# Kernel optimization log

Hardware: AMD Instinct MI355X
Metric: run time of the kernel (lower is better)

Reference implementation:

```python
import jax, jax.numpy as jnp
import numpy as np

B, S, D, H = 2, 2048, 1024, 16
HD = D // H               # head_dim = input_size / num_heads
STEPS = 1                 # update_steps_max extra Hopfield update steps
LN_EPS = 1e-5
SCALING = 1.0 / np.sqrt(HD)  # beta = 1/sqrt(head_dim)


def layernorm(x, g, b):
    m = x.mean(-1, keepdims=True)
    v = ((x - m) ** 2).mean(-1, keepdims=True)
    return (x - m) * jax.lax.rsqrt(v + LN_EPS) * g + b


def setup_inputs() -> dict:
    key = jax.random.key(0)
    ks = jax.random.split(key, 9)
    s = 0.02
    f32 = jnp.float32
    return {
        "data": jax.random.normal(ks[0], (B, S, D), f32),
        # affine LayerNorm params (stored / state / projection patterns)
        "g_k": jnp.ones((D,), f32), "b_k": jnp.zeros((D,), f32),
        "g_q": jnp.ones((D,), f32), "b_q": jnp.zeros((D,), f32),
        "g_v": jnp.ones((D,), f32), "b_v": jnp.zeros((D,), f32),
        # in-projections (q/k/v) and out-projection of HopfieldCore
        "Wq": jax.random.normal(ks[1], (D, D), f32) * s, "bq": jnp.zeros((D,), f32),
        "Wk": jax.random.normal(ks[2], (D, D), f32) * s, "bk": jnp.zeros((D,), f32),
        "Wv": jax.random.normal(ks[3], (D, D), f32) * s, "bv": jnp.zeros((D,), f32),
        "Wo": jax.random.normal(ks[4], (D, D), f32) * s, "bo": jnp.zeros((D,), f32),
    }


def reference(data, g_k, b_k, g_q, b_q, g_v, b_v,
              Wq, bq, Wk, bk, Wv, bv, Wo, bo):
    # single input tensor used as stored / state / projection pattern
    xk = layernorm(data, g_k, b_k)   # stored pattern  -> keys
    xq = layernorm(data, g_q, b_q)   # state pattern   -> queries
    xv = layernorm(data, g_v, b_v)   # pattern proj    -> values

    split = lambda t: t.reshape(B, S, H, HD).transpose(0, 2, 1, 3)  # [B,H,S,HD]
    q = split(xq @ Wq + bq)
    k = split(xk @ Wk + bk)
    v = split(xv @ Wv + bv)

    def assoc(q):  # xi = softmax(beta * q K^T)
        return jax.nn.softmax(
            jnp.einsum('bhqd,bhkd->bhqk', q, k) * SCALING, axis=-1)

    xi = assoc(q)
    for _ in range(STEPS):           # iterative Hopfield update: q <- xi K
        q = jnp.einsum('bhqk,bhkd->bhqd', xi, k)
        xi = assoc(q)

    out = jnp.einsum('bhqk,bhkd->bhqd', xi, v)        # retrieve with values
    out = out.transpose(0, 2, 1, 3).reshape(B, S, D)  # merge heads
    return out @ Wo + bo
```

## Files before the change

kernel.cpp:

```cpp
#include <hip/hip_runtime.h>
#include <hip/hip_bf16.h>

#define B_  2
#define S_  2048
#define D_  1024
#define H_  16
#define HD_ 64
#define M_  4096


typedef __attribute__((ext_vector_type(8))) short short8;
typedef __attribute__((ext_vector_type(4))) float f32x4;
typedef __attribute__((ext_vector_type(16))) float f32x16;

#define CE_ 0.1803368801111204f

typedef __attribute__((address_space(1))) const unsigned GU;
typedef __attribute__((address_space(3))) unsigned LU;
static __device__ __forceinline__ void glds16(const void* g, void* l){
  __builtin_amdgcn_global_load_lds((GU*)g, (LU*)l, 16, 0, 0);
}

static __device__ __forceinline__ unsigned short f2bfc(float f){
  union{float f; unsigned u;} c; c.f = f;
  return (unsigned short)((c.u + 0x8000u) >> 16);
}
static __device__ __forceinline__ unsigned pk2bf(float a, float b){
  union{float f; unsigned u;} ca, cb; ca.f=a; cb.f=b;
  return __builtin_amdgcn_perm(cb.u + 0x8000u, ca.u + 0x8000u, 0x07060302u);
}
static __device__ __forceinline__ unsigned pk2bft(float a, float b){
  union{float f; unsigned u;} ca, cb; ca.f=a; cb.f=b;
  return __builtin_amdgcn_perm(cb.u, ca.u, 0x07060302u);
}
static __device__ __forceinline__ short8 mk8(unsigned x0, unsigned x1,
                                             unsigned x2, unsigned x3){
  union{ unsigned u[4]; short8 s; } t;
  t.u[0]=x0; t.u[1]=x1; t.u[2]=x2; t.u[3]=x3; return t.s;
}
static __device__ __forceinline__ void plswap(unsigned &x, unsigned &y){
  auto r = __builtin_amdgcn_permlane32_swap(x, y, false, false);
  x = (unsigned)r[0]; y = (unsigned)r[1];
}

__global__ __launch_bounds__(256) void prep_kernel(
  const float* __restrict__ data,
  const float* __restrict__ Wq, const float* __restrict__ Wk,
  const float* __restrict__ Wv, const float* __restrict__ Wo,
  const float* __restrict__ gq, const float* __restrict__ gk, const float* __restrict__ gv,
  const float* __restrict__ blq, const float* __restrict__ blk, const float* __restrict__ blv,
  const float* __restrict__ bpq, const float* __restrict__ bpk, const float* __restrict__ bpv,
  unsigned short* __restrict__ WT, unsigned short* __restrict__ xhat,
  float* __restrict__ bf)
{
  __shared__ unsigned short tile[64][72];
  __shared__ float red[4][64];
  int bid = blockIdx.x, t = threadIdx.x;
  if (bid < 1024){
    int z = bid >> 8, rem = bid & 255;
    int k0 = (rem>>4)*64, n0 = (rem&15)*64;
    const float* W = (z==0)?Wq:(z==1)?Wk:(z==2)?Wv:Wo;
    const float* g = (z==0)?gq:(z==1)?gk:(z==2)?gv:(const float*)0;
    unsigned short* out = WT + ((size_t)z<<20);
    {
      int kr = t>>2, c16 = (t&3)*16;
      float gs = g ? g[k0+kr]*((z==0)?CE_:1.0f) : 1.0f;
      const float* src = W + (size_t)(k0+kr)*D_ + n0 + c16;
      float4 w0 = *(const float4*)(src);
      float4 w1 = *(const float4*)(src+4);
      float4 w2 = *(const float4*)(src+8);
      float4 w3 = *(const float4*)(src+12);
      unsigned* tp = (unsigned*)&tile[kr][c16];
      tp[0]=pk2bf(w0.x*gs,w0.y*gs); tp[1]=pk2bf(w0.z*gs,w0.w*gs);
      tp[2]=pk2bf(w1.x*gs,w1.y*gs); tp[3]=pk2bf(w1.z*gs,w1.w*gs);
      tp[4]=pk2bf(w2.x*gs,w2.y*gs); tp[5]=pk2bf(w2.z*gs,w2.w*gs);
      tp[6]=pk2bf(w3.x*gs,w3.y*gs); tp[7]=pk2bf(w3.z*gs,w3.w*gs);
    }
    __syncthreads();
    {
      int nr = t>>2, kc = (t&3)*16;
      union { uint4 v[2]; unsigned short u[16]; } st;
      #pragma unroll
      for (int i=0;i<16;i++) st.u[i] = tile[kc+i][nr];
      unsigned short* dst = out + (size_t)(n0+nr)*D_ + k0 + kc;
      *(uint4*)(dst)     = st.v[0];
      *(uint4*)(dst + 8) = st.v[1];
    }
  } else if (bid < 2048){
    int row = (bid-1024)*4 + (t>>6);
    int l = t & 63;
    const float4* xr = (const float4*)(data + (size_t)row*D_);
    float4 v[4];
    float s = 0.f, ss = 0.f;
    #pragma unroll
    for (int i=0;i<4;i++){
      v[i] = xr[l + 64*i];
      s  += v[i].x+v[i].y+v[i].z+v[i].w;
      ss += v[i].x*v[i].x+v[i].y*v[i].y+v[i].z*v[i].z+v[i].w*v[i].w;
    }
    #pragma unroll
    for (int m=1;m<64;m<<=1){ s += __shfl_xor(s, m, 64); ss += __shfl_xor(ss, m, 64); }
    float me = s*(1.0f/D_);
    float var = ss*(1.0f/D_) - me*me;
    float rs = rsqrtf(var + 1e-5f);
    float nm = -me*rs;
    unsigned short* xo = xhat + (size_t)row*D_;
    #pragma unroll
    for (int i=0;i<4;i++){
      uint2 pk;
      pk.x = pk2bf(fmaf(v[i].x,rs,nm), fmaf(v[i].y,rs,nm));
      pk.y = pk2bf(fmaf(v[i].z,rs,nm), fmaf(v[i].w,rs,nm));
      *(uint2*)(xo + 4*l + 256*i) = pk;
    }
  } else {
    int idx = bid - 2048;
    int z = idx >> 4, xb = idx & 15;
    const float* W  = (z==0)?Wq:(z==1)?Wk:Wv;
    const float* bl = (z==0)?blq:(z==1)?blk:blv;
    const float* bp = (z==0)?bpq:(z==1)?bpk:bpv;
    int nl = t & 63, kg = t >> 6;
    int n = xb*64 + nl;
    float acc = 0.f;
    for (int k = kg*256; k < (kg+1)*256; k++)
      acc += bl[k] * W[(size_t)k*D_ + n];
    red[kg][nl] = acc;
    __syncthreads();
    if (t < 64){
      int nn = xb*64 + t;
      float v = red[0][t]+red[1][t]+red[2][t]+red[3][t] + bp[nn];
      bf[z*D_ + nn] = (z==0) ? v*CE_ : v;
    }
  }
}

__global__ __launch_bounds__(256) void gemm_qkv(
  const unsigned short* __restrict__ xhat,
  const unsigned short* __restrict__ WT,
  const float* __restrict__ biasf,
  unsigned short* __restrict__ qv, unsigned short* __restrict__ kb,
  unsigned short* __restrict__ kT, unsigned short* __restrict__ vT)
{
  int z = blockIdx.z;
  const unsigned short* Bt = WT + ((size_t)z<<20);
  const float* bias = biasf + z*D_;
  unsigned short* oN = (z==0)?qv:(z==1)?kb:(unsigned short*)0;
  unsigned short* oT = (z==0)?(unsigned short*)0:(z==1)?kT:vT;

  __shared__ __align__(16) unsigned short As[128*32];
  __shared__ __align__(16) unsigned short Bs[128*32];
  int tid = threadIdx.x, w = tid>>6, l = tid&63;
  int m0 = blockIdx.x*128, n0 = blockIdx.y*128;
  int wr = (w>>1)*64, wc = (w&1)*64;
  int lr = l&15, qd = l>>4;

  const unsigned short* gA = xhat + (size_t)(m0 + w*32 + (l>>2))*D_ + (l&3)*8;
  const unsigned short* gB = Bt   + (size_t)(n0 + w*32 + (l>>2))*D_ + (l&3)*8;
  unsigned short* lA0 = &As[(w*32)*32];
  unsigned short* lA1 = &As[(w*32+16)*32];
  unsigned short* lB0 = &Bs[(w*32)*32];
  unsigned short* lB1 = &Bs[(w*32+16)*32];

  const f32x4 fz = {0.f,0.f,0.f,0.f};
  f32x4 acc[4][4];
  #pragma unroll
  for (int i=0;i<4;i++)
    #pragma unroll
    for (int j=0;j<4;j++) acc[i][j] = fz;

  for (int kk=0; kk<D_; kk+=32){
    __syncthreads();
    glds16(gA + kk,                 lA0);
    glds16(gA + kk + (size_t)16*D_, lA1);
    glds16(gB + kk,                 lB0);
    glds16(gB + kk + (size_t)16*D_, lB1);
    __syncthreads();
    short8 af[4], bfr[4];
    #pragma unroll
    for (int i=0;i<4;i++) af[i]  = *(const short8*)(As + (wr + i*16 + lr)*32 + qd*8);
    #pragma unroll
    for (int j=0;j<4;j++) bfr[j] = *(const short8*)(Bs + (wc + j*16 + lr)*32 + qd*8);
    #pragma unroll
    for (int i=0;i<4;i++)
      #pragma unroll
      for (int j=0;j<4;j++)
        acc[i][j] = __builtin_amdgcn_mfma_f32_16x16x32_bf16(af[i], bfr[j], acc[i][j], 0, 0, 0);
  }

  #pragma unroll
  for (int j=0;j<4;j++){
    int n = n0 + wc + j*16 + lr;
    float bias_n = bias[n];
    #pragma unroll
    for (int i=0;i<4;i++){
      int mb = m0 + wr + i*16 + qd*4;
      float v0 = acc[i][j][0] + bias_n;
      float v1 = acc[i][j][1] + bias_n;
      float v2 = acc[i][j][2] + bias_n;
      float v3 = acc[i][j][3] + bias_n;
      if (oN){
        oN[(size_t)(mb+0)*D_ + n] = f2bfc(v0);
        oN[(size_t)(mb+1)*D_ + n] = f2bfc(v1);
        oN[(size_t)(mb+2)*D_ + n] = f2bfc(v2);
        oN[(size_t)(mb+3)*D_ + n] = f2bfc(v3);
      }
      if (oT){
        int bb = mb >> 11, sI = mb & (S_-1);
        int hh = n >> 6,  dd = n & 63;
        uint2 pk; pk.x = pk2bf(v0, v1); pk.y = pk2bf(v2, v3);
        *(uint2*)(oT + (size_t)((bb*H_ + hh)*HD_ + dd)*S_ + sI) = pk;
      }
    }
  }
}

__global__ __launch_bounds__(256) void gemm_out(
  const unsigned short* __restrict__ A,
  const unsigned short* __restrict__ Bt,
  const float* __restrict__ bo,
  float* __restrict__ Cf)
{
  __shared__ __align__(16) unsigned short As[128*32];
  __shared__ __align__(16) unsigned short Bs[128*32];
  int tid = threadIdx.x, w = tid>>6, l = tid&63;
  int m0 = blockIdx.x*128, n0 = blockIdx.y*128;
  int wr = (w>>1)*64, wc = (w&1)*64;
  int lr = l&15, qd = l>>4;

  const unsigned short* gA = A  + (size_t)(m0 + w*32 + (l>>2))*D_ + (l&3)*8;
  const unsigned short* gB = Bt + (size_t)(n0 + w*32 + (l>>2))*D_ + (l&3)*8;
  unsigned short* lA0 = &As[(w*32)*32];
  unsigned short* lA1 = &As[(w*32+16)*32];
  unsigned short* lB0 = &Bs[(w*32)*32];
  unsigned short* lB1 = &Bs[(w*32+16)*32];

  const f32x4 fz = {0.f,0.f,0.f,0.f};
  f32x4 acc[4][4];
  #pragma unroll
  for (int i=0;i<4;i++)
    #pragma unroll
    for (int j=0;j<4;j++) acc[i][j] = fz;

  for (int kk=0; kk<D_; kk+=32){
    __syncthreads();
    glds16(gA + kk,                 lA0);
    glds16(gA + kk + (size_t)16*D_, lA1);
    glds16(gB + kk,                 lB0);
    glds16(gB + kk + (size_t)16*D_, lB1);
    __syncthreads();
    short8 af[4], bfr[4];
    #pragma unroll
    for (int i=0;i<4;i++) af[i]  = *(const short8*)(As + (wr + i*16 + lr)*32 + qd*8);
    #pragma unroll
    for (int j=0;j<4;j++) bfr[j] = *(const short8*)(Bs + (wc + j*16 + lr)*32 + qd*8);
    #pragma unroll
    for (int i=0;i<4;i++)
      #pragma unroll
      for (int j=0;j<4;j++)
        acc[i][j] = __builtin_amdgcn_mfma_f32_16x16x32_bf16(af[i], bfr[j], acc[i][j], 0, 0, 0);
  }

  #pragma unroll
  for (int j=0;j<4;j++){
    int n = n0 + wc + j*16 + lr;
    float bias_n = bo[n];
    #pragma unroll
    for (int i=0;i<4;i++){
      int mb = m0 + wr + i*16 + qd*4;
      Cf[(size_t)(mb+0)*D_ + n] = acc[i][j][0] + bias_n;
      Cf[(size_t)(mb+1)*D_ + n] = acc[i][j][1] + bias_n;
      Cf[(size_t)(mb+2)*D_ + n] = acc[i][j][2] + bias_n;
      Cf[(size_t)(mb+3)*D_ + n] = acc[i][j][3] + bias_n;
    }
  }
}

__global__ __launch_bounds__(256) void attn_fused(
  unsigned short* __restrict__ QO,
  const unsigned short* __restrict__ K,
  const unsigned short* __restrict__ KT,
  const unsigned short* __restrict__ VT)
{
  int qt = blockIdx.x;
  int h  = blockIdx.y;
  int b  = qt >> 4;
  int bh = b*H_ + h;
  int tid = threadIdx.x, w = tid>>6, l = tid&63;
  int lq = l & 31;
  int hi = l >> 5;
  int r8 = tid>>3, c8 = (tid&7)*8;
  int swzw = (r8&7)<<3;
  int swzr = (lq&7)<<3;

  __shared__ __align__(16) unsigned short sK[64*64];
  __shared__ __align__(16) unsigned short sV[64*64];

  const f32x16 fz16 = {0.f,0.f,0.f,0.f,0.f,0.f,0.f,0.f,
                       0.f,0.f,0.f,0.f,0.f,0.f,0.f,0.f};
  const short8 ones = {(short)0x3F80,(short)0x3F80,(short)0x3F80,(short)0x3F80,
                       (short)0x3F80,(short)0x3F80,(short)0x3F80,(short)0x3F80};

  const unsigned short* Qb = QO + (size_t)(qt*128 + w*32 + lq)*D_ + h*64;
  short8 qf[4];
  #pragma unroll
  for (int d=0; d<4; d++)
    qf[d] = *(const short8*)(Qb + d*16 + hi*8);

  const unsigned short* Khead = K + (size_t)(b*S_)*D_ + h*64;
  const unsigned short* Vh0 = KT + (size_t)bh*HD_*S_;
  const unsigned short* Vh1 = VT + (size_t)bh*HD_*S_;

  uint4 kr0, kr1, vr0, vr1;
  kr0 = *(const uint4*)(Khead + (size_t)(r8   )*D_ + c8);
  kr1 = *(const uint4*)(Khead + (size_t)(r8+32)*D_ + c8);
  vr0 = *(const uint4*)(Vh0 + (size_t)(r8   )*S_ + c8);
  vr1 = *(const uint4*)(Vh0 + (size_t)(r8+32)*S_ + c8);

  #pragma unroll 1
  for (int phase=0; phase<2; phase++){
    const unsigned short* Vhead = phase ? Vh1 : Vh0;
    f32x16 oacc0 = fz16, oacc1 = fz16, lacc = fz16;

    for (int kt=0; kt<S_; kt+=64){
      __syncthreads();
      *(uint4*)(&sK[(size_t)(r8   )*64 + (c8 ^ swzw)]) = kr0;
      *(uint4*)(&sK[(size_t)(r8+32)*64 + (c8 ^ swzw)]) = kr1;
      *(uint4*)(&sV[(size_t)(r8   )*64 + (c8 ^ swzw)]) = vr0;
      *(uint4*)(&sV[(size_t)(r8+32)*64 + (c8 ^ swzw)]) = vr1;
      __syncthreads();

      {
        int nkt = kt + 64;
        const unsigned short* Vn = Vhead;
        if (nkt >= S_){ nkt = 0; Vn = Vh1; }
        kr0 = *(const uint4*)(Khead + (size_t)(nkt+r8   )*D_ + c8);
        kr1 = *(const uint4*)(Khead + (size_t)(nkt+r8+32)*D_ + c8);
        vr0 = *(const uint4*)(Vn + (size_t)(r8   )*S_ + nkt + c8);
        vr1 = *(const uint4*)(Vn + (size_t)(r8+32)*S_ + nkt + c8);
      }

      f32x16 sc0 = fz16, sc1 = fz16;
      #pragma unroll
      for (int ds_=0; ds_<4; ds_++){
        short8 ka0 = *(const short8*)(&sK[(size_t)(lq   )*64 + ((ds_*16 + hi*8) ^ swzr)]);
        short8 ka1 = *(const short8*)(&sK[(size_t)(lq+32)*64 + ((ds_*16 + hi*8) ^ swzr)]);
        sc0 = __builtin_amdgcn_mfma_f32_32x32x16_bf16(ka0, qf[ds_], sc0, 0,0,0);
        sc1 = __builtin_amdgcn_mfma_f32_32x32x16_bf16(ka1, qf[ds_], sc1, 0,0,0);
      }

      float p0[16], p1[16];
      #pragma unroll
      for (int i=0;i<16;i++){
        p0[i] = __builtin_amdgcn_exp2f(sc0[i]);
        p1[i] = __builtin_amdgcn_exp2f(sc1[i]);
      }
      short8 pf[4];
      {
        unsigned a0,a1,b0,b1;
        a0=pk2bft(p0[0],p0[1]);   a1=pk2bft(p0[2],p0[3]);
        b0=pk2bft(p0[4],p0[5]);   b1=pk2bft(p0[6],p0[7]);
        plswap(a0,b0); plswap(a1,b1);
        pf[0] = mk8(a0,a1,b0,b1);
        a0=pk2bft(p0[8],p0[9]);   a1=pk2bft(p0[10],p0[11]);
        b0=pk2bft(p0[12],p0[13]); b1=pk2bft(p0[14],p0[15]);
        plswap(a0,b0); plswap(a1,b1);
        pf[1] = mk8(a0,a1,b0,b1);
        a0=pk2bft(p1[0],p1[1]);   a1=pk2bft(p1[2],p1[3]);
        b0=pk2bft(p1[4],p1[5]);   b1=pk2bft(p1[6],p1[7]);
        plswap(a0,b0); plswap(a1,b1);
        pf[2] = mk8(a0,a1,b0,b1);
        a0=pk2bft(p1[8],p1[9]);   a1=pk2bft(p1[10],p1[11]);
        b0=pk2bft(p1[12],p1[13]); b1=pk2bft(p1[14],p1[15]);
        plswap(a0,b0); plswap(a1,b1);
        pf[3] = mk8(a0,a1,b0,b1);
      }

      #pragma unroll
      for (int ks=0; ks<4; ks++){
        short8 va0 = *(const short8*)(&sV[(size_t)(lq   )*64 + ((ks*16 + hi*8) ^ swzr)]);
        short8 va1 = *(const short8*)(&sV[(size_t)(lq+32)*64 + ((ks*16 + hi*8) ^ swzr)]);
        oacc0 = __builtin_amdgcn_mfma_f32_32x32x16_bf16(va0, pf[ks], oacc0, 0,0,0);
        oacc1 = __builtin_amdgcn_mfma_f32_32x32x16_bf16(va1, pf[ks], oacc1, 0,0,0);
        lacc  = __builtin_amdgcn_mfma_f32_32x32x16_bf16(ones, pf[ks], lacc, 0,0,0);
      }
    }

    if (phase==0){
      float iv = CE_ * __builtin_amdgcn_rcpf(lacc[0]);
      unsigned a0,a1,b0,b1;
      a0=pk2bf(oacc0[0]*iv, oacc0[1]*iv);   a1=pk2bf(oacc0[2]*iv, oacc0[3]*iv);
      b0=pk2bf(oacc0[4]*iv, oacc0[5]*iv);   b1=pk2bf(oacc0[6]*iv, oacc0[7]*iv);
      plswap(a0,b0); plswap(a1,b1);
      qf[0] = mk8(a0,a1,b0,b1);
      a0=pk2bf(oacc0[8]*iv, oacc0[9]*iv);   a1=pk2bf(oacc0[10]*iv, oacc0[11]*iv);
      b0=pk2bf(oacc0[12]*iv, oacc0[13]*iv); b1=pk2bf(oacc0[14]*iv, oacc0[15]*iv);
      plswap(a0,b0); plswap(a1,b1);
      qf[1] = mk8(a0,a1,b0,b1);
      a0=pk2bf(oacc1[0]*iv, oacc1[1]*iv);   a1=pk2bf(oacc1[2]*iv, oacc1[3]*iv);
      b0=pk2bf(oacc1[4]*iv, oacc1[5]*iv);   b1=pk2bf(oacc1[6]*iv, oacc1[7]*iv);
      plswap(a0,b0); plswap(a1,b1);
      qf[2] = mk8(a0,a1,b0,b1);
      a0=pk2bf(oacc1[8]*iv, oacc1[9]*iv);   a1=pk2bf(oacc1[10]*iv, oacc1[11]*iv);
      b0=pk2bf(oacc1[12]*iv, oacc1[13]*iv); b1=pk2bf(oacc1[14]*iv, oacc1[15]*iv);
      plswap(a0,b0); plswap(a1,b1);
      qf[3] = mk8(a0,a1,b0,b1);
    } else {
      float iv = __builtin_amdgcn_rcpf(lacc[0]);
      unsigned short* Ob = QO + (size_t)(qt*128 + w*32 + lq)*D_ + h*64 + hi*4;
      #pragma unroll
      for (int g=0; g<4; g++){
        uint2 pk;
        pk.x = pk2bf(oacc0[4*g+0]*iv, oacc0[4*g+1]*iv);
        pk.y = pk2bf(oacc0[4*g+2]*iv, oacc0[4*g+3]*iv);
        *(uint2*)(Ob + g*8) = pk;
        pk.x = pk2bf(oacc1[4*g+0]*iv, oacc1[4*g+1]*iv);
        pk.y = pk2bf(oacc1[4*g+2]*iv, oacc1[4*g+3]*iv);
        *(uint2*)(Ob + 32 + g*8) = pk;
      }
    }
  }
}

extern "C" void kernel_launch(void* const* d_in, const int* in_sizes, int n_in,
                              void* d_out, int out_size, void* d_ws, size_t ws_size,
                              hipStream_t stream){
  const float* data = (const float*)d_in[0];
  const float* g_k  = (const float*)d_in[1];
  const float* b_k  = (const float*)d_in[2];
  const float* g_q  = (const float*)d_in[3];
  const float* b_q  = (const float*)d_in[4];
  const float* g_v  = (const float*)d_in[5];
  const float* b_v  = (const float*)d_in[6];
  const float* Wq   = (const float*)d_in[7];
  const float* bq   = (const float*)d_in[8];
  const float* Wk   = (const float*)d_in[9];
  const float* bk   = (const float*)d_in[10];
  const float* Wv   = (const float*)d_in[11];
  const float* bv   = (const float*)d_in[12];
  const float* Wo   = (const float*)d_in[13];
  const float* bo   = (const float*)d_in[14];
  float* out = (float*)d_out;

  char* ws = (char*)d_ws;
  const size_t MB = (size_t)1<<20;
  unsigned short* q    = (unsigned short*)(ws);
  unsigned short* kb   = (unsigned short*)(ws + 8*MB);
  unsigned short* WT   = (unsigned short*)(ws + 16*MB);
  unsigned short* WTo  = WT + ((size_t)3<<20);
  unsigned short* xhat = (unsigned short*)(ws + 24*MB);
  float*          bfld = (float*)(ws + 32*MB);
  unsigned short* vT   = (unsigned short*)d_out;
  unsigned short* kT   = (unsigned short*)((char*)d_out + 8*MB);

  dim3 gb(256);
  prep_kernel<<<dim3(2096), gb, 0, stream>>>(data,
                                             Wq, Wk, Wv, Wo, g_q, g_k, g_v,
                                             b_q, b_k, b_v, bq, bk, bv,
                                             WT, xhat, bfld);
  gemm_qkv<<<dim3(32,8,3), gb, 0, stream>>>(xhat, WT, bfld, q, kb, kT, vT);
  attn_fused<<<dim3(32, H_), gb, 0, stream>>>(q, kb, kT, vT);
  gemm_out<<<dim3(32,8), gb, 0, stream>>>(q, WTo, bo, out);
}
```

Measured before the change: 256.5 us.

## Split attention key range across warp pairs and load K/V tiles directly into LDS

The attention kernel now uses 64-query blocks (twice as many blocks) where two warp pairs each process half of a 128-key tile, and partial outputs and denominators are reduced through shared memory. K/V tiles are loaded with global_load_lds into swizzled LDS, replacing register staging. The ones-matrix MFMA for the row sum is replaced by a scalar sum plus a cross-lane shuffle, and s_setprio brackets the MFMA sections. This aims to raise occupancy and parallelism and to cut MFMA work, at the cost of an extra LDS reduction and more barriers, and without register prefetch overlap.

After: 251.9 us. No clear change (-1.8%).

```diff
diff --git a/kernel.cpp b/kernel.cpp
--- a/kernel.cpp
+++ b/kernel.cpp
@@ -274,7 +274,7 @@
   }
 }
 
-__global__ __launch_bounds__(256) void attn_fused(
+__global__ __launch_bounds__(256, 4) void attn_fused(
   unsigned short* __restrict__ QO,
   const unsigned short* __restrict__ K,
   const unsigned short* __restrict__ KT,
@@ -282,76 +282,95 @@
 {
   int qt = blockIdx.x;
   int h  = blockIdx.y;
-  int b  = qt >> 4;
+  int b  = qt >> 5;
   int bh = b*H_ + h;
   int tid = threadIdx.x, w = tid>>6, l = tid&63;
-  int lq = l & 31;
-  int hi = l >> 5;
-  int r8 = tid>>3, c8 = (tid&7)*8;
-  int swzw = (r8&7)<<3;
-  int swzr = (lq&7)<<3;
-
-  __shared__ __align__(16) unsigned short sK[64*64];
-  __shared__ __align__(16) unsigned short sV[64*64];
+  int wq = w & 1, wk = w >> 1;
+  int lq = l & 31, hi = l >> 5;
+  int swzr = (lq & 7) << 3;
+
+  __shared__ __align__(16) unsigned short smem[16384];
+  unsigned short* sK = smem;
+  unsigned short* sV = smem + 8192;
 
   const f32x16 fz16 = {0.f,0.f,0.f,0.f,0.f,0.f,0.f,0.f,
                        0.f,0.f,0.f,0.f,0.f,0.f,0.f,0.f};
-  const short8 ones = {(short)0x3F80,(short)0x3F80,(short)0x3F80,(short)0x3F80,
-                       (short)0x3F80,(short)0x3F80,(short)0x3F80,(short)0x3F80};
-
-  const unsigned short* Qb = QO + (size_t)(qt*128 + w*32 + lq)*D_ + h*64;
+
+  const unsigned short* Qb = QO + (size_t)(qt*64 + wq*32 + lq)*D_ + h*64;
   short8 qf[4];
   #pragma unroll
-  for (int d=0; d<4; d++)
-    qf[d] = *(const short8*)(Qb + d*16 + hi*8);
+  for (int d=0; d<4; d++) qf[d] = *(const short8*)(Qb + d*16 + hi*8);
 
   const unsigned short* Khead = K + (size_t)(b*S_)*D_ + h*64;
   const unsigned short* Vh0 = KT + (size_t)bh*HD_*S_;
   const unsigned short* Vh1 = VT + (size_t)bh*HD_*S_;
 
-  uint4 kr0, kr1, vr0, vr1;
-  kr0 = *(const uint4*)(Khead + (size_t)(r8   )*D_ + c8);
-  kr1 = *(const uint4*)(Khead + (size_t)(r8+32)*D_ + c8);
-  vr0 = *(const uint4*)(Vh0 + (size_t)(r8   )*S_ + c8);
-  vr1 = *(const uint4*)(Vh0 + (size_t)(r8+32)*S_ + c8);
+  int seg = w*4;
+  int kcol = ((l&7)*8) ^ (((l>>3)&7)*8);
+  const unsigned short* gKb = Khead + (size_t)(seg*8 + (l>>3))*D_ + kcol;
+  int vrE = seg*4 + (l>>4);
+  int vcE = ((l&15)*8) ^ (((l>>4)&7)*8);
+  int vcO = ((l&15)*8) ^ ((((l>>4)+4)&7)*8);
+
+  unsigned short* lK0 = sK + (seg+0)*512;
+  unsigned short* lK1 = sK + (seg+1)*512;
+  unsigned short* lK2 = sK + (seg+2)*512;
+  unsigned short* lK3 = sK + (seg+3)*512;
+  unsigned short* lV0 = sV + (seg+0)*512;
+  unsigned short* lV1 = sV + (seg+1)*512;
+  unsigned short* lV2 = sV + (seg+2)*512;
+  unsigned short* lV3 = sV + (seg+3)*512;
 
   #pragma unroll 1
   for (int phase=0; phase<2; phase++){
     const unsigned short* Vhead = phase ? Vh1 : Vh0;
-    f32x16 oacc0 = fz16, oacc1 = fz16, lacc = fz16;
-
-    for (int kt=0; kt<S_; kt+=64){
+    const unsigned short* gK  = gKb;
+    const unsigned short* gV0 = Vhead + (size_t)(vrE  )*S_ + vcE;
+    const unsigned short* gV1 = Vhead + (size_t)(vrE+4)*S_ + vcO;
+
+    f32x16 oacc0 = fz16, oacc1 = fz16;
+    float den = 0.f;
+
+    #pragma unroll 1
+    for (int ss=0; ss<16; ss++){
       __syncthreads();
-      *(uint4*)(&sK[(size_t)(r8   )*64 + (c8 ^ swzw)]) = kr0;
-      *(uint4*)(&sK[(size_t)(r8+32)*64 + (c8 ^ swzw)]) = kr1;
-      *(uint4*)(&sV[(size_t)(r8   )*64 + (c8 ^ swzw)]) = vr0;
-      *(uint4*)(&sV[(size_t)(r8+32)*64 + (c8 ^ swzw)]) = vr1;
+      glds16(gK,          lK0);
+      glds16(gK +  8*D_,  lK1);
+      glds16(gK + 16*D_,  lK2);
+      glds16(gK + 24*D_,  lK3);
+      glds16(gV0,         lV0);
+      glds16(gV1,         lV1);
+      glds16(gV0 + 8*S_,  lV2);
+      glds16(gV1 + 8*S_,  lV3);
       __syncthreads();
-
-      {
-        int nkt = kt + 64;
-        const unsigned short* Vn = Vhead;
-        if (nkt >= S_){ nkt = 0; Vn = Vh1; }
-        kr0 = *(const uint4*)(Khead + (size_t)(nkt+r8   )*D_ + c8);
-        kr1 = *(const uint4*)(Khead + (size_t)(nkt+r8+32)*D_ + c8);
-        vr0 = *(const uint4*)(Vn + (size_t)(r8   )*S_ + nkt + c8);
-        vr1 = *(const uint4*)(Vn + (size_t)(r8+32)*S_ + nkt + c8);
-      }
+      gK  += 128*D_;
+      gV0 += 128;
+      gV1 += 128;
 
       f32x16 sc0 = fz16, sc1 = fz16;
-      #pragma unroll
-      for (int ds_=0; ds_<4; ds_++){
-        short8 ka0 = *(const short8*)(&sK[(size_t)(lq   )*64 + ((ds_*16 + hi*8) ^ swzr)]);
-        short8 ka1 = *(const short8*)(&sK[(size_t)(lq+32)*64 + ((ds_*16 + hi*8) ^ swzr)]);
-        sc0 = __builtin_amdgcn_mfma_f32_32x32x16_bf16(ka0, qf[ds_], sc0, 0,0,0);
-        sc1 = __builtin_amdgcn_mfma_f32_32x32x16_bf16(ka1, qf[ds_], sc1, 0,0,0);
-      }
+      __builtin_amdgcn_s_setprio(1);
+      #pragma unroll
+      for (int d4=0; d4<4; d4++){
+        int rc = (d4*16 + hi*8) ^ swzr;
+        short8 ka0 = *(const short8*)(&sK[(size_t)(wk*64 + lq     )*64 + rc]);
+        short8 ka1 = *(const short8*)(&sK[(size_t)(wk*64 + lq + 32)*64 + rc]);
+        sc0 = __builtin_amdgcn_mfma_f32_32x32x16_bf16(ka0, qf[d4], sc0, 0,0,0);
+        sc1 = __builtin_amdgcn_mfma_f32_32x32x16_bf16(ka1, qf[d4], sc1, 0,0,0);
+      }
+      __builtin_amdgcn_s_setprio(0);
 
       float p0[16], p1[16];
       #pragma unroll
       for (int i=0;i<16;i++){
         p0[i] = __builtin_amdgcn_exp2f(sc0[i]);
         p1[i] = __builtin_amdgcn_exp2f(sc1[i]);
+      }
+      {
+        float t0 = ((p0[0]+p0[1])+(p0[2]+p0[3])) + ((p0[4]+p0[5])+(p0[6]+p0[7]));
+        float t1 = ((p0[8]+p0[9])+(p0[10]+p0[11])) + ((p0[12]+p0[13])+(p0[14]+p0[15]));
+        float t2 = ((p1[0]+p1[1])+(p1[2]+p1[3])) + ((p1[4]+p1[5])+(p1[6]+p1[7]));
+        float t3 = ((p1[8]+p1[9])+(p1[10]+p1[11])) + ((p1[12]+p1[13])+(p1[14]+p1[15]));
+        den += (t0+t1)+(t2+t3);
       }
       short8 pf[4];
       {
@@ -374,48 +393,83 @@
         pf[3] = mk8(a0,a1,b0,b1);
       }
 
+      __builtin_amdgcn_s_setprio(1);
       #pragma unroll
       for (int ks=0; ks<4; ks++){
-        short8 va0 = *(const short8*)(&sV[(size_t)(lq   )*64 + ((ks*16 + hi*8) ^ swzr)]);
-        short8 va1 = *(const short8*)(&sV[(size_t)(lq+32)*64 + ((ks*16 + hi*8) ^ swzr)]);
+        int rc = (wk*64 + ks*16 + hi*8) ^ swzr;
+        short8 va0 = *(const short8*)(&sV[(size_t)(lq     )*128 + rc]);
+        short8 va1 = *(const short8*)(&sV[(size_t)(lq + 32)*128 + rc]);
         oacc0 = __builtin_amdgcn_mfma_f32_32x32x16_bf16(va0, pf[ks], oacc0, 0,0,0);
         oacc1 = __builtin_amdgcn_mfma_f32_32x32x16_bf16(va1, pf[ks], oacc1, 0,0,0);
-        lacc  = __builtin_amdgcn_mfma_f32_32x32x16_bf16(ones, pf[ks], lacc, 0,0,0);
-      }
-    }
-
-    if (phase==0){
-      float iv = CE_ * __builtin_amdgcn_rcpf(lacc[0]);
-      unsigned a0,a1,b0,b1;
-      a0=pk2bf(oacc0[0]*iv, oacc0[1]*iv);   a1=pk2bf(oacc0[2]*iv, oacc0[3]*iv);
-      b0=pk2bf(oacc0[4]*iv, oacc0[5]*iv);   b1=pk2bf(oacc0[6]*iv, oacc0[7]*iv);
-      plswap(a0,b0); plswap(a1,b1);
-      qf[0] = mk8(a0,a1,b0,b1);
-      a0=pk2bf(oacc0[8]*iv, oacc0[9]*iv);   a1=pk2bf(oacc0[10]*iv, oacc0[11]*iv);
-      b0=pk2bf(oacc0[12]*iv, oacc0[13]*iv); b1=pk2bf(oacc0[14]*iv, oacc0[15]*iv);
-      plswap(a0,b0); plswap(a1,b1);
-      qf[1] = mk8(a0,a1,b0,b1);
-      a0=pk2bf(oacc1[0]*iv, oacc1[1]*iv);   a1=pk2bf(oacc1[2]*iv, oacc1[3]*iv);
-      b0=pk2bf(oacc1[4]*iv, oacc1[5]*iv);   b1=pk2bf(oacc1[6]*iv, oacc1[7]*iv);
-      plswap(a0,b0); plswap(a1,b1);
-      qf[2] = mk8(a0,a1,b0,b1);
-      a0=pk2bf(oacc1[8]*iv, oacc1[9]*iv);   a1=pk2bf(oacc1[10]*iv, oacc1[11]*iv);
-      b0=pk2bf(oacc1[12]*iv, oacc1[13]*iv); b1=pk2bf(oacc1[14]*iv, oacc1[15]*iv);
-      plswap(a0,b0); plswap(a1,b1);
-      qf[3] = mk8(a0,a1,b0,b1);
-    } else {
-      float iv = __builtin_amdgcn_rcpf(lacc[0]);
-      unsigned short* Ob = QO + (size_t)(qt*128 + w*32 + lq)*D_ + h*64 + hi*4;
-      #pragma unroll
-      for (int g=0; g<4; g++){
-        uint2 pk;
-        pk.x = pk2bf(oacc0[4*g+0]*iv, oacc0[4*g+1]*iv);
-        pk.y = pk2bf(oacc0[4*g+2]*iv, oacc0[4*g+3]*iv);
-        *(uint2*)(Ob + g*8) = pk;
-        pk.x = pk2bf(oacc1[4*g+0]*iv, oacc1[4*g+1]*iv);
-        pk.y = pk2bf(oacc1[4*g+2]*iv, oacc1[4*g+3]*iv);
-        *(uint2*)(Ob + 32 + g*8) = pk;
-      }
+      }
+      __builtin_amdgcn_s_setprio(0);
+    }
+
+    den += __shfl_xor(den, 32, 64);
+
+    float* fb = (float*)smem;
+    int cb = wq*2112;
+    __syncthreads();
+    if (wk==1){
+      #pragma unroll
+      for (int i=0;i<16;i++){
+        fb[cb + i*64 + l]      = oacc0[i];
+        fb[cb + (16+i)*64 + l] = oacc1[i];
+      }
+      fb[cb + 2048 + l] = den;
+    }
+    __syncthreads();
+    if (wk==0){
+      #pragma unroll
+      for (int i=0;i<16;i++){
+        oacc0[i] += fb[cb + i*64 + l];
+        oacc1[i] += fb[cb + (16+i)*64 + l];
+      }
+      den += fb[cb + 2048 + l];
+      if (phase==0){
+        float iv = CE_ * __builtin_amdgcn_rcpf(den);
+        unsigned a0,a1,b0,b1;
+        a0=pk2bf(oacc0[0]*iv, oacc0[1]*iv);   a1=pk2bf(oacc0[2]*iv, oacc0[3]*iv);
+        b0=pk2bf(oacc0[4]*iv, oacc0[5]*iv);   b1=pk2bf(oacc0[6]*iv, oacc0[7]*iv);
+        plswap(a0,b0); plswap(a1,b1);
+        qf[0] = mk8(a0,a1,b0,b1);
+        a0=pk2bf(oacc0[8]*iv, oacc0[9]*iv);   a1=pk2bf(oacc0[10]*iv, oacc0[11]*iv);
+        b0=pk2bf(oacc0[12]*iv, oacc0[13]*iv); b1=pk2bf(oacc0[14]*iv, oacc0[15]*iv);
+        plswap(a0,b0); plswap(a1,b1);
+        qf[1] = mk8(a0,a1,b0,b1);
+        a0=pk2bf(oacc1[0]*iv, oacc1[1]*iv);   a1=pk2bf(oacc1[2]*iv, oacc1[3]*iv);
+        b0=pk2bf(oacc1[4]*iv, oacc1[5]*iv);   b1=pk2bf(oacc1[6]*iv, oacc1[7]*iv);
+        plswap(a0,b0); plswap(a1,b1);
+        qf[2] = mk8(a0,a1,b0,b1);
+        a0=pk2bf(oacc1[8]*iv, oacc1[9]*iv);   a1=pk2bf(oacc1[10]*iv, oacc1[11]*iv);
+        b0=pk2bf(oacc1[12]*iv, oacc1[13]*iv); b1=pk2bf(oacc1[14]*iv, oacc1[15]*iv);
+        plswap(a0,b0); plswap(a1,b1);
+        qf[3] = mk8(a0,a1,b0,b1);
+        unsigned short* qsh = smem + 12288 + wq*2048;
+        #pragma unroll
+        for (int d=0; d<4; d++)
+          *(short8*)(qsh + d*512 + l*8) = qf[d];
+      } else {
+        float iv = __builtin_amdgcn_rcpf(den);
+        unsigned short* Ob = QO + (size_t)(qt*64 + wq*32 + lq)*D_ + h*64 + hi*4;
+        #pragma unroll
+        for (int g=0; g<4; g++){
+          uint2 pk;
+          pk.x = pk2bf(oacc0[4*g+0]*iv, oacc0[4*g+1]*iv);
+          pk.y = pk2bf(oacc0[4*g+2]*iv, oacc0[4*g+3]*iv);
+          *(uint2*)(Ob + g*8) = pk;
+          pk.x = pk2bf(oacc1[4*g+0]*iv, oacc1[4*g+1]*iv);
+          pk.y = pk2bf(oacc1[4*g+2]*iv, oacc1[4*g+3]*iv);
+          *(uint2*)(Ob + 32 + g*8) = pk;
+        }
+      }
+    }
+    __syncthreads();
+    if (phase==0 && wk==1){
+      unsigned short* qsh = smem + 12288 + wq*2048;
+      #pragma unroll
+      for (int d=0; d<4; d++)
+        qf[d] = *(const short8*)(qsh + d*512 + l*8);
     }
   }
 }
@@ -457,6 +511,6 @@
                                              b_q, b_k, b_v, bq, bk, bv,
                                              WT, xhat, bfld);
   gemm_qkv<<<dim3(32,8,3), gb, 0, stream>>>(xhat, WT, bfld, q, kb, kT, vT);
-  attn_fused<<<dim3(32, H_), gb, 0, stream>>>(q, kb, kT, vT);
+  attn_fused<<<dim3(64, H_), gb, 0, stream>>>(q, kb, kT, vT);
   gemm_out<<<dim3(32,8), gb, 0, stream>>>(q, WTo, bo, out);
 }
```
